# Optimization experiments

Measured on AMD Instinct MI355X. Metric: run time of the kernel, lower is better.

## Reference

```python
import jax, jax.numpy as jnp
import numpy as np

N, F, H, G = 4096, 256, 8, 128  # atoms, filters, heads, groups
D = F // H  # head dim = 32


def setup_inputs() -> dict:
    key = jax.random.key(0)
    ks = jax.random.split(key, 12)
    x = jax.random.normal(ks[0], (N, F), dtype=jnp.float32)
    # sorted group ids in [0, G): block_diag over unique-count blocks == equality mask on sorted ids
    seg = jnp.sort(jax.random.randint(ks[1], (N,), 0, G, dtype=jnp.int32))
    elem_index = jnp.stack([jnp.arange(N, dtype=jnp.int32), seg])  # [2, N]
    s = 1.0 / np.sqrt(F)
    def lin(k):
        kw, kb = jax.random.split(k)
        return (jax.random.normal(kw, (F, F), dtype=jnp.float32) * s,
                jnp.zeros((F,), dtype=jnp.float32))
    Wq, bq = lin(ks[2]); Wk, bk = lin(ks[3]); Wv, bv = lin(ks[4])
    Wo1, bo1 = lin(ks[5]); Wo2, bo2 = lin(ks[6])
    return {"x": x, "elem_index": elem_index,
            "Wq": Wq, "bq": bq, "Wk": Wk, "bk": bk, "Wv": Wv, "bv": bv,
            "Wo1": Wo1, "bo1": bo1, "Wo2": Wo2, "bo2": bo2}


def reference(x, elem_index, Wq, bq, Wk, bk, Wv, bv, Wo1, bo1, Wo2, bo2):
    n = x.shape[0]
    # projections -> [H, N, D]
    q = (x @ Wq.T + bq).reshape(n, H, D).transpose(1, 0, 2)
    k = (x @ Wk.T + bk).reshape(n, H, D).transpose(1, 0, 2)
    v = (x @ Wv.T + bv).reshape(n, H, D).transpose(1, 0, 2)
    attn = jnp.einsum('hnd,hmd->hnm', q, k)          # [H, N, N]
    attn = jax.nn.silu(attn)                          # attn_act = activation() in source
    seg = elem_index[1]
    mask = (seg[:, None] == seg[None, :]).astype(attn.dtype)  # block-diagonal (sorted ids)
    attn = attn * mask
    out = jnp.einsum('hnm,hmd->hnd', attn, v)        # [H, N, D]
    out = out.transpose(1, 0, 2).reshape(n, F)       # [N, F]
    out = out @ Wo1.T + bo1
    out = jax.ops.segment_sum(out, seg, num_segments=G)  # scatter sum by group -> [G, F]
    out = out @ Wo2.T + bo2
    return jax.nn.silu(out)
```

## Files before the change

kernel.cpp:

```cpp
#include <hip/hip_runtime.h>
#include <math.h>

#define NATOMS 4096
#define FDIM   256
#define NHEAD  8
#define DHEAD  32
#define NGRP   128

typedef __bf16 bf16x8 __attribute__((ext_vector_type(8)));
typedef float  floatx4 __attribute__((ext_vector_type(4)));

__device__ __forceinline__ float silu_f(float x) {
    return x / (1.0f + __expf(-x));
}

__device__ __forceinline__ bf16x8 cvt8(const float* __restrict__ p) {
    float4 f0 = *(const float4*)p;
    float4 f1 = *(const float4*)(p + 4);
    bf16x8 r;
    r[0] = (__bf16)f0.x; r[1] = (__bf16)f0.y; r[2] = (__bf16)f0.z; r[3] = (__bf16)f0.w;
    r[4] = (__bf16)f1.x; r[5] = (__bf16)f1.y; r[6] = (__bf16)f1.z; r[7] = (__bf16)f1.w;
    return r;
}

__global__ __launch_bounds__(256) void k1_qkv_a2(
    const float* __restrict__ x, const int* __restrict__ seg,
    const float* __restrict__ Wq, const float* __restrict__ Wk, const float* __restrict__ Wv,
    const float* __restrict__ bq, const float* __restrict__ bk, const float* __restrict__ bv,
    const float* __restrict__ Wo1, const float* __restrict__ bo1,
    const float* __restrict__ Wo2,
    float* __restrict__ qkv, float* __restrict__ A2, float* __restrict__ c1,
    float* __restrict__ cntf, int* __restrict__ off)
{
    __shared__ float As[32][33];
    __shared__ float Bs[32][33];
    __shared__ int   segs[NATOMS];

    const int tid = threadIdx.x;
    const int bid = blockIdx.x;

    if (bid < 512) {
        int lane = tid & 63;
        int ww = tid >> 6;
        int wrow = ww >> 1, wcol = ww & 1;
        int tm = bid & 63;
        int tn = bid >> 6;
        int m_base = tm * 64 + wrow * 32;
        int n_base = tn * 96 + wcol * 48;

        int l15 = lane & 15;
        int quad = lane >> 4;
        int kq = quad * 8;

        floatx4 acc[2][3] = {};

        const float* arow0 = x + (size_t)(m_base + l15) * 256 + kq;
        const float* arow1 = arow0 + 16 * 256;
        const float* brow[3];
        const float* bias[3];
#pragma unroll
        for (int ni = 0; ni < 3; ++ni) {
            int col = n_base + ni * 16 + l15;
            int w = col >> 8, c = col & 255;
            const float* W = (w == 0) ? Wq : (w == 1) ? Wk : Wv;
            brow[ni] = W + (size_t)c * 256 + kq;
            bias[ni] = ((w == 0) ? bq : (w == 1) ? bk : bv) + c;
        }

#pragma unroll
        for (int ks = 0; ks < 8; ++ks) {
            int ko = ks * 32;
            bf16x8 a0 = cvt8(arow0 + ko);
            bf16x8 a1 = cvt8(arow1 + ko);
#pragma unroll
            for (int ni = 0; ni < 3; ++ni) {
                bf16x8 b = cvt8(brow[ni] + ko);
                acc[0][ni] = __builtin_amdgcn_mfma_f32_16x16x32_bf16(a0, b, acc[0][ni], 0, 0, 0);
                acc[1][ni] = __builtin_amdgcn_mfma_f32_16x16x32_bf16(a1, b, acc[1][ni], 0, 0, 0);
            }
        }

#pragma unroll
        for (int mi = 0; mi < 2; ++mi) {
#pragma unroll
            for (int ni = 0; ni < 3; ++ni) {
                int col = n_base + ni * 16 + l15;
                int w = col >> 8, c = col & 255;
                float bb = *bias[ni];
                float* outp = qkv + (size_t)w * ((size_t)NATOMS * FDIM) + c;
#pragma unroll
                for (int r = 0; r < 4; ++r) {
                    int row = m_base + mi * 16 + quad * 4 + r;
                    outp[(size_t)row * FDIM] = acc[mi][ni][r] + bb;
                }
            }
        }
    } else if (bid < 576) {
        int t = bid - 512;
        int i0 = (t >> 3) * 32;
        int j0 = (t & 7) * 32;
        bool do_c1 = (t & 7) == 0;
        int tx = tid & 15;
        int ty = tid >> 4;
        int lm = tid >> 3;
        int lk = (tid & 7) << 2;

        float acc[2][2] = {};
        float c1acc = 0.0f;

        for (int kt = 0; kt < 256; kt += 32) {
            const float4 av = *(const float4*)(Wo2 + (size_t)(i0 + lm) * 256 + kt + lk);
            const float4 bv = *(const float4*)(Wo1 + (size_t)(kt + lm) * 256 + j0 + lk);
            As[lk + 0][lm] = av.x; As[lk + 1][lm] = av.y;
            As[lk + 2][lm] = av.z; As[lk + 3][lm] = av.w;
            Bs[lm][lk + 0] = bv.x; Bs[lm][lk + 1] = bv.y;
            Bs[lm][lk + 2] = bv.z; Bs[lm][lk + 3] = bv.w;
            __syncthreads();

#pragma unroll
            for (int kk = 0; kk < 32; ++kk) {
                float a0 = As[kk][ty * 2], a1 = As[kk][ty * 2 + 1];
                float b0 = Bs[kk][tx * 2], b1 = Bs[kk][tx * 2 + 1];
                acc[0][0] = fmaf(a0, b0, acc[0][0]);
                acc[0][1] = fmaf(a0, b1, acc[0][1]);
                acc[1][0] = fmaf(a1, b0, acc[1][0]);
                acc[1][1] = fmaf(a1, b1, acc[1][1]);
            }
            if (do_c1) {
                float4 bb = *(const float4*)(bo1 + kt + lk);
                c1acc = fmaf(As[lk + 0][lm], bb.x, c1acc);
                c1acc = fmaf(As[lk + 1][lm], bb.y, c1acc);
                c1acc = fmaf(As[lk + 2][lm], bb.z, c1acc);
                c1acc = fmaf(As[lk + 3][lm], bb.w, c1acc);
            }
            __syncthreads();
        }

#pragma unroll
        for (int i = 0; i < 2; ++i)
#pragma unroll
            for (int j = 0; j < 2; ++j)
                A2[(size_t)(i0 + ty * 2 + i) * 256 + j0 + tx * 2 + j] = acc[i][j];

        if (do_c1) {
            c1acc += __shfl_xor(c1acc, 1, 8);
            c1acc += __shfl_xor(c1acc, 2, 8);
            c1acc += __shfl_xor(c1acc, 4, 8);
            if ((tid & 7) == 0) c1[i0 + lm] = c1acc;
        }
    } else {
        for (int i = tid; i < NATOMS; i += 256) segs[i] = seg[i];
        __syncthreads();
        if (tid < NGRP) {
            int g = tid;
            auto lb = [&](int val) {
                int lo = 0, hi = NATOMS;
                while (lo < hi) {
                    int mid = (lo + hi) >> 1;
                    if (segs[mid] < val) lo = mid + 1; else hi = mid;
                }
                return lo;
            };
            int a = lb(g);
            int b = lb(g + 1);
            off[g] = a;
            if (g == NGRP - 1) off[NGRP] = NATOMS;
            cntf[g] = (float)(b - a);
        }
    }
}

__global__ __launch_bounds__(256) void attn_kernel(
    const float* __restrict__ qkv, const int* __restrict__ off,
    float* __restrict__ Ysum)
{
    int g = blockIdx.x, h = blockIdx.y;
    int base = off[g];
    int end  = off[g + 1];
    base = min(max(base, 0), NATOMS);
    end  = min(max(end, base), NATOMS);
    int n = end - base;

    __shared__ float4 qt4[64 * 8];
    __shared__ float4 vt4[32 * 8];
    __shared__ float  wred[8][32];
    __shared__ float  w[32];
    __shared__ float  red[8][32];

    int tid = threadIdx.x;
    int jj = tid & 31;
    int iq = tid >> 5;
    int d = tid & 31;
    int r = tid >> 5;

    const float* q = qkv;
    const float* k = qkv + (size_t)NATOMS * FDIM;
    const float* v = qkv + 2 * (size_t)NATOMS * FDIM;

    const float4* q4 = (const float4*)(q + (size_t)base * FDIM) + h * 8;
    const float4* k4 = (const float4*)(k + (size_t)base * FDIM) + h * 8;
    const float4* v4 = (const float4*)(v + (size_t)base * FDIM) + h * 8;

    float accY = 0.0f;

    for (int j0 = 0; j0 < n; j0 += 32) {
        int jt_n = min(32, n - j0);
        __syncthreads();
        for (int idx = tid; idx < jt_n * 8; idx += 256)
            vt4[idx] = v4[(size_t)(j0 + (idx >> 3)) * 64 + (idx & 7)];

        float4 kr[8];
        {
            int jrow = (jj < jt_n) ? (j0 + jj) : j0;
#pragma unroll
            for (int c = 0; c < 8; ++c) kr[c] = k4[(size_t)jrow * 64 + c];
        }

        float wpart = 0.0f;
        for (int i0 = 0; i0 < n; i0 += 64) {
            int it_n = min(64, n - i0);
            __syncthreads();
            for (int idx = tid; idx < it_n * 8; idx += 256)
                qt4[idx] = q4[(size_t)(i0 + (idx >> 3)) * 64 + (idx & 7)];
            __syncthreads();
            if (jj < jt_n) {
                for (int ii = iq; ii < it_n; ii += 8) {
                    const float4* qr = &qt4[ii * 8];
                    float s = 0.0f;
#pragma unroll
                    for (int c = 0; c < 8; ++c) {
                        float4 a = qr[c];
                        s = fmaf(a.x, kr[c].x, s);
                        s = fmaf(a.y, kr[c].y, s);
                        s = fmaf(a.z, kr[c].z, s);
                        s = fmaf(a.w, kr[c].w, s);
                    }
                    wpart += silu_f(s);
                }
            }
        }
        wred[iq][jj] = wpart;
        __syncthreads();
        if (tid < 32) {
            float s = 0.0f;
#pragma unroll
            for (int rr = 0; rr < 8; ++rr) s += wred[rr][tid];
            w[tid] = s;
        }
        __syncthreads();
        const float* vts = (const float*)vt4;
        for (int j = r; j < jt_n; j += 8)
            accY = fmaf(w[j], vts[j * 32 + d], accY);
    }

    red[r][d] = accY;
    __syncthreads();
    if (r == 0) {
        float s = 0.0f;
#pragma unroll
        for (int rr = 0; rr < 8; ++rr) s += red[rr][d];
        Ysum[(size_t)g * FDIM + h * DHEAD + d] = s;
    }
}

__global__ __launch_bounds__(256) void k3_tail(
    const float* __restrict__ Ysum, const float* __restrict__ A2,
    const float* __restrict__ c1, const float* __restrict__ bo2,
    const float* __restrict__ cntf, float* __restrict__ out)
{
    __shared__ float As[32][17];
    __shared__ float Bs[32][33];

    int tid = threadIdx.x;
    int bm = (blockIdx.x >> 3) * 16;
    int bn = (blockIdx.x & 7) * 32;
    int tx = tid & 15;
    int ty = tid >> 4;

    float acc0 = 0.0f, acc1 = 0.0f;

    for (int kt = 0; kt < 256; kt += 32) {
        if (tid < 128) {
            int row = tid >> 3, kq = (tid & 7) << 2;
            const float4 av = *(const float4*)(Ysum + (size_t)(bm + row) * 256 + kt + kq);
            As[kq + 0][row] = av.x; As[kq + 1][row] = av.y;
            As[kq + 2][row] = av.z; As[kq + 3][row] = av.w;
        }
        {
            int row = tid >> 3, kq = (tid & 7) << 2;
            const float4 bv = *(const float4*)(A2 + (size_t)(bn + row) * 256 + kt + kq);
            Bs[kq + 0][row] = bv.x; Bs[kq + 1][row] = bv.y;
            Bs[kq + 2][row] = bv.z; Bs[kq + 3][row] = bv.w;
        }
        __syncthreads();

#pragma unroll
        for (int kk = 0; kk < 32; ++kk) {
            float a = As[kk][ty];
            acc0 = fmaf(a, Bs[kk][tx * 2], acc0);
            acc1 = fmaf(a, Bs[kk][tx * 2 + 1], acc1);
        }
        __syncthreads();
    }

    int m = bm + ty;
    float cnt = cntf[m];
    int n0 = bn + tx * 2;
    float v0 = silu_f(acc0 + cnt * c1[n0] + bo2[n0]);
    float v1 = silu_f(acc1 + cnt * c1[n0 + 1] + bo2[n0 + 1]);
    out[(size_t)m * 256 + n0] = v0;
    out[(size_t)m * 256 + n0 + 1] = v1;
}

extern "C" void kernel_launch(void* const* d_in, const int* in_sizes, int n_in,
                              void* d_out, int out_size, void* d_ws, size_t ws_size,
                              hipStream_t stream) {
    const float* x    = (const float*)d_in[0];
    const int*   eidx = (const int*)  d_in[1];
    const float* Wq   = (const float*)d_in[2];
    const float* bq   = (const float*)d_in[3];
    const float* Wk   = (const float*)d_in[4];
    const float* bk   = (const float*)d_in[5];
    const float* Wv   = (const float*)d_in[6];
    const float* bv   = (const float*)d_in[7];
    const float* Wo1  = (const float*)d_in[8];
    const float* bo1  = (const float*)d_in[9];
    const float* Wo2  = (const float*)d_in[10];
    const float* bo2  = (const float*)d_in[11];
    float* out = (float*)d_out;

    const int* seg = eidx + NATOMS;

    const size_t NF = (size_t)NATOMS * FDIM;
    const size_t GF = (size_t)NGRP * FDIM;

    float* qkv  = (float*)d_ws;
    float* Ysum = qkv + 3 * NF;
    float* A2   = Ysum + GF;
    float* c1   = A2 + 256 * 256;
    float* cntf = c1 + 256;
    int*   off  = (int*)(cntf + NGRP);

    k1_qkv_a2<<<577, 256, 0, stream>>>(x, seg, Wq, Wk, Wv, bq, bk, bv,
                                       Wo1, bo1, Wo2, qkv, A2, c1, cntf, off);

    dim3 gattn(NGRP, NHEAD);
    attn_kernel<<<gattn, 256, 0, stream>>>(qkv, off, Ysum);

    k3_tail<<<64, 256, 0, stream>>>(Ysum, A2, c1, bo2, cntf, out);
}
```

Before: 131.7 us.

## Fuse QKV, attention and tail kernels into one launch with atomic flags

Merges the three kernel launches into a single kernel. Role is chosen by block index, and stages are ordered with agent-scope atomic counters and spin-waits rather than kernel boundaries. Attention work is packed four group/head jobs per block so all blocks can be co-resident. This removes inter-kernel launch gaps and lets the A2 work overlap the attention stage. The costs are less attention parallelism per block and a risk of deadlock or races: the F_READY flag is never reset between calls, so on repeated launches producer blocks can signal before the counters are cleared.

```diff
diff --git a/kernel.cpp b/kernel.cpp
--- a/kernel.cpp
+++ b/kernel.cpp
@@ -6,6 +6,20 @@
 #define NHEAD  8
 #define DHEAD  32
 #define NGRP   128
+
+#define NB_QKV   512
+#define NB_A2    64
+#define B_OFF    (NB_QKV + NB_A2)
+#define B_ATTN0  (B_OFF + 1)
+#define NB_ATTN  256
+#define B_TAIL0  (B_ATTN0 + NB_ATTN)
+#define NB_TAIL  64
+#define NB_ALL   (B_TAIL0 + NB_TAIL)
+
+#define F_READY  0
+#define F_QKV    16
+#define F_A2     32
+#define F_ATTN   48
 
 typedef __bf16 bf16x8 __attribute__((ext_vector_type(8)));
 typedef float  floatx4 __attribute__((ext_vector_type(4)));
@@ -23,23 +37,46 @@
     return r;
 }
 
-__global__ __launch_bounds__(256) void k1_qkv_a2(
+__device__ __forceinline__ void wait_eq(int* p, int val) {
+    while (__hip_atomic_load(p, __ATOMIC_ACQUIRE, __HIP_MEMORY_SCOPE_AGENT) != val)
+        __builtin_amdgcn_s_sleep(2);
+}
+
+__device__ __forceinline__ void signal_add(int* p) {
+    __hip_atomic_fetch_add(p, 1, __ATOMIC_RELEASE, __HIP_MEMORY_SCOPE_AGENT);
+}
+
+struct SM {
+    union {
+        struct {
+            float4 qt4[64 * 8];
+            float4 vt4[32 * 8];
+            float  wred[8][32];
+            float  w[32];
+            float  red[8][32];
+        } a;
+        int segs[NATOMS];
+        struct { float As[32][33]; float Bs[32][33]; } g;
+        struct { float As[32][17]; float Bs[32][33]; } t;
+    };
+};
+
+__global__ __launch_bounds__(256, 4) void fused_all(
     const float* __restrict__ x, const int* __restrict__ seg,
     const float* __restrict__ Wq, const float* __restrict__ Wk, const float* __restrict__ Wv,
     const float* __restrict__ bq, const float* __restrict__ bk, const float* __restrict__ bv,
     const float* __restrict__ Wo1, const float* __restrict__ bo1,
-    const float* __restrict__ Wo2,
-    float* __restrict__ qkv, float* __restrict__ A2, float* __restrict__ c1,
-    float* __restrict__ cntf, int* __restrict__ off)
+    const float* __restrict__ Wo2, const float* __restrict__ bo2,
+    float* __restrict__ out,
+    float* __restrict__ qkv, float* __restrict__ Ysum,
+    float* __restrict__ A2, float* __restrict__ c1,
+    float* __restrict__ cntf, int* __restrict__ off, int* __restrict__ flags)
 {
-    __shared__ float As[32][33];
-    __shared__ float Bs[32][33];
-    __shared__ int   segs[NATOMS];
-
+    __shared__ SM sm;
     const int tid = threadIdx.x;
     const int bid = blockIdx.x;
 
-    if (bid < 512) {
+    if (bid < NB_QKV) {
         int lane = tid & 63;
         int ww = tid >> 6;
         int wrow = ww >> 1, wcol = ww & 1;
@@ -95,8 +132,12 @@
                 }
             }
         }
-    } else if (bid < 576) {
-        int t = bid - 512;
+        __threadfence();
+        __syncthreads();
+        if (tid == 0) { wait_eq(&flags[F_READY], 1); signal_add(&flags[F_QKV]); }
+
+    } else if (bid < B_OFF) {
+        int t = bid - NB_QKV;
         int i0 = (t >> 3) * 32;
         int j0 = (t & 7) * 32;
         bool do_c1 = (t & 7) == 0;
@@ -111,16 +152,16 @@
         for (int kt = 0; kt < 256; kt += 32) {
             const float4 av = *(const float4*)(Wo2 + (size_t)(i0 + lm) * 256 + kt + lk);
             const float4 bv = *(const float4*)(Wo1 + (size_t)(kt + lm) * 256 + j0 + lk);
-            As[lk + 0][lm] = av.x; As[lk + 1][lm] = av.y;
-            As[lk + 2][lm] = av.z; As[lk + 3][lm] = av.w;
-            Bs[lm][lk + 0] = bv.x; Bs[lm][lk + 1] = bv.y;
-            Bs[lm][lk + 2] = bv.z; Bs[lm][lk + 3] = bv.w;
+            sm.g.As[lk + 0][lm] = av.x; sm.g.As[lk + 1][lm] = av.y;
+            sm.g.As[lk + 2][lm] = av.z; sm.g.As[lk + 3][lm] = av.w;
+            sm.g.Bs[lm][lk + 0] = bv.x; sm.g.Bs[lm][lk + 1] = bv.y;
+            sm.g.Bs[lm][lk + 2] = bv.z; sm.g.Bs[lm][lk + 3] = bv.w;
             __syncthreads();
 
 #pragma unroll
             for (int kk = 0; kk < 32; ++kk) {
-                float a0 = As[kk][ty * 2], a1 = As[kk][ty * 2 + 1];
-                float b0 = Bs[kk][tx * 2], b1 = Bs[kk][tx * 2 + 1];
+                float a0 = sm.g.As[kk][ty * 2], a1 = sm.g.As[kk][ty * 2 + 1];
+                float b0 = sm.g.Bs[kk][tx * 2], b1 = sm.g.Bs[kk][tx * 2 + 1];
                 acc[0][0] = fmaf(a0, b0, acc[0][0]);
                 acc[0][1] = fmaf(a0, b1, acc[0][1]);
                 acc[1][0] = fmaf(a1, b0, acc[1][0]);
@@ -128,10 +169,10 @@
             }
             if (do_c1) {
                 float4 bb = *(const float4*)(bo1 + kt + lk);
-                c1acc = fmaf(As[lk + 0][lm], bb.x, c1acc);
-                c1acc = fmaf(As[lk + 1][lm], bb.y, c1acc);
-                c1acc = fmaf(As[lk + 2][lm], bb.z, c1acc);
-                c1acc = fmaf(As[lk + 3][lm], bb.w, c1acc);
+                c1acc = fmaf(sm.g.As[lk + 0][lm], bb.x, c1acc);
+                c1acc = fmaf(sm.g.As[lk + 1][lm], bb.y, c1acc);
+                c1acc = fmaf(sm.g.As[lk + 2][lm], bb.z, c1acc);
+                c1acc = fmaf(sm.g.As[lk + 3][lm], bb.w, c1acc);
             }
             __syncthreads();
         }
@@ -148,8 +189,15 @@
             c1acc += __shfl_xor(c1acc, 4, 8);
             if ((tid & 7) == 0) c1[i0 + lm] = c1acc;
         }
-    } else {
-        for (int i = tid; i < NATOMS; i += 256) segs[i] = seg[i];
+        __threadfence();
+        __syncthreads();
+        if (tid == 0) { wait_eq(&flags[F_READY], 1); signal_add(&flags[F_A2]); }
+
+    } else if (bid == B_OFF) {
+        if (tid == 1) flags[F_QKV] = 0;
+        if (tid == 2) flags[F_A2] = 0;
+        if (tid == 3) flags[F_ATTN] = 0;
+        for (int i = tid; i < NATOMS; i += 256) sm.segs[i] = seg[i];
         __syncthreads();
         if (tid < NGRP) {
             int g = tid;
@@ -157,7 +205,7 @@
                 int lo = 0, hi = NATOMS;
                 while (lo < hi) {
                     int mid = (lo + hi) >> 1;
-                    if (segs[mid] < val) lo = mid + 1; else hi = mid;
+                    if (sm.segs[mid] < val) lo = mid + 1; else hi = mid;
                 }
                 return lo;
             };
@@ -167,149 +215,149 @@
             if (g == NGRP - 1) off[NGRP] = NATOMS;
             cntf[g] = (float)(b - a);
         }
+        __threadfence();
+        __syncthreads();
+        if (tid == 0)
+            __hip_atomic_store(&flags[F_READY], 1, __ATOMIC_RELEASE, __HIP_MEMORY_SCOPE_AGENT);
+
+    } else if (bid < B_TAIL0) {
+        if (tid == 0) wait_eq(&flags[F_QKV], NB_QKV);
+        __syncthreads();
+
+        const float* q = qkv;
+        const float* k = qkv + (size_t)NATOMS * FDIM;
+        const float* v = qkv + 2 * (size_t)NATOMS * FDIM;
+
+        int jj = tid & 31;
+        int iq = tid >> 5;
+        int d = tid & 31;
+        int r = tid >> 5;
+
+        for (int t = 0; t < 4; ++t) {
+            int job = (bid - B_ATTN0) * 4 + t;
+            int g = job >> 3, h = job & 7;
+
+            int base = off[g];
+            int end  = off[g + 1];
+            base = min(max(base, 0), NATOMS);
+            end  = min(max(end, base), NATOMS);
+            int n = end - base;
+
+            const float4* q4 = (const float4*)(q + (size_t)base * FDIM) + h * 8;
+            const float4* k4 = (const float4*)(k + (size_t)base * FDIM) + h * 8;
+            const float4* v4 = (const float4*)(v + (size_t)base * FDIM) + h * 8;
+
+            float accY = 0.0f;
+
+            for (int j0 = 0; j0 < n; j0 += 32) {
+                int jt_n = min(32, n - j0);
+                __syncthreads();
+                for (int idx = tid; idx < jt_n * 8; idx += 256)
+                    sm.a.vt4[idx] = v4[(size_t)(j0 + (idx >> 3)) * 64 + (idx & 7)];
+
+                float4 kr[8];
+                {
+                    int jrow = (jj < jt_n) ? (j0 + jj) : j0;
+#pragma unroll
+                    for (int c = 0; c < 8; ++c) kr[c] = k4[(size_t)jrow * 64 + c];
+                }
+
+                float wpart = 0.0f;
+                for (int i0 = 0; i0 < n; i0 += 64) {
+                    int it_n = min(64, n - i0);
+                    __syncthreads();
+                    for (int idx = tid; idx < it_n * 8; idx += 256)
+                        sm.a.qt4[idx] = q4[(size_t)(i0 + (idx >> 3)) * 64 + (idx & 7)];
+                    __syncthreads();
+                    if (jj < jt_n) {
+                        for (int ii = iq; ii < it_n; ii += 8) {
+                            const float4* qr = &sm.a.qt4[ii * 8];
+                            float s = 0.0f;
+#pragma unroll
+                            for (int c = 0; c < 8; ++c) {
+                                float4 a = qr[c];
+                                s = fmaf(a.x, kr[c].x, s);
+                                s = fmaf(a.y, kr[c].y, s);
+                                s = fmaf(a.z, kr[c].z, s);
+                                s = fmaf(a.w, kr[c].w, s);
+                            }
+                            wpart += silu_f(s);
+                        }
+                    }
+                }
+                sm.a.wred[iq][jj] = wpart;
+                __syncthreads();
+                if (tid < 32) {
+                    float s = 0.0f;
+#pragma unroll
+                    for (int rr = 0; rr < 8; ++rr) s += sm.a.wred[rr][tid];
+                    sm.a.w[tid] = s;
+                }
+                __syncthreads();
+                const float* vts = (const float*)sm.a.vt4;
+                for (int j = r; j < jt_n; j += 8)
+                    accY = fmaf(sm.a.w[j], vts[j * 32 + d], accY);
+            }
+
+            sm.a.red[r][d] = accY;
+            __syncthreads();
+            if (r == 0) {
+                float s = 0.0f;
+#pragma unroll
+                for (int rr = 0; rr < 8; ++rr) s += sm.a.red[rr][d];
+                Ysum[(size_t)g * FDIM + h * DHEAD + d] = s;
+            }
+            __syncthreads();
+        }
+        __threadfence();
+        __syncthreads();
+        if (tid == 0) signal_add(&flags[F_ATTN]);
+
+    } else {
+        if (tid == 0) {
+            wait_eq(&flags[F_ATTN], NB_ATTN);
+            wait_eq(&flags[F_A2], NB_A2);
+        }
+        __syncthreads();
+
+        int blk = bid - B_TAIL0;
+        int bm = (blk >> 3) * 16;
+        int bn = (blk & 7) * 32;
+        int tx = tid & 15;
+        int ty = tid >> 4;
+
+        float acc0 = 0.0f, acc1 = 0.0f;
+
+        for (int kt = 0; kt < 256; kt += 32) {
+            if (tid < 128) {
+                int row = tid >> 3, kq = (tid & 7) << 2;
+                const float4 av = *(const float4*)(Ysum + (size_t)(bm + row) * 256 + kt + kq);
+                sm.t.As[kq + 0][row] = av.x; sm.t.As[kq + 1][row] = av.y;
+                sm.t.As[kq + 2][row] = av.z; sm.t.As[kq + 3][row] = av.w;
+            }
+            {
+                int row = tid >> 3, kq = (tid & 7) << 2;
+                const float4 bv = *(const float4*)(A2 + (size_t)(bn + row) * 256 + kt + kq);
+                sm.t.Bs[kq + 0][row] = bv.x; sm.t.Bs[kq + 1][row] = bv.y;
+                sm.t.Bs[kq + 2][row] = bv.z; sm.t.Bs[kq + 3][row] = bv.w;
+            }
+            __syncthreads();
+
+#pragma unroll
+            for (int kk = 0; kk < 32; ++kk) {
+                float a = sm.t.As[kk][ty];
+                acc0 = fmaf(a, sm.t.Bs[kk][tx * 2], acc0);
+                acc1 = fmaf(a, sm.t.Bs[kk][tx * 2 + 1], acc1);
+            }
+            __syncthreads();
+        }
+
+        int m = bm + ty;
+        float cnt = cntf[m];
+        int n0 = bn + tx * 2;
+        out[(size_t)m * 256 + n0]     = silu_f(acc0 + cnt * c1[n0] + bo2[n0]);
+        out[(size_t)m * 256 + n0 + 1] = silu_f(acc1 + cnt * c1[n0 + 1] + bo2[n0 + 1]);
     }
-}
-
-__global__ __launch_bounds__(256) void attn_kernel(
-    const float* __restrict__ qkv, const int* __restrict__ off,
-    float* __restrict__ Ysum)
-{
-    int g = blockIdx.x, h = blockIdx.y;
-    int base = off[g];
-    int end  = off[g + 1];
-    base = min(max(base, 0), NATOMS);
-    end  = min(max(end, base), NATOMS);
-    int n = end - base;
-
-    __shared__ float4 qt4[64 * 8];
-    __shared__ float4 vt4[32 * 8];
-    __shared__ float  wred[8][32];
-    __shared__ float  w[32];
-    __shared__ float  red[8][32];
-
-    int tid = threadIdx.x;
-    int jj = tid & 31;
-    int iq = tid >> 5;
-    int d = tid & 31;
-    int r = tid >> 5;
-
-    const float* q = qkv;
-    const float* k = qkv + (size_t)NATOMS * FDIM;
-    const float* v = qkv + 2 * (size_t)NATOMS * FDIM;
-
-    const float4* q4 = (const float4*)(q + (size_t)base * FDIM) + h * 8;
-    const float4* k4 = (const float4*)(k + (size_t)base * FDIM) + h * 8;
-    const float4* v4 = (const float4*)(v + (size_t)base * FDIM) + h * 8;
-
-    float accY = 0.0f;
-
-    for (int j0 = 0; j0 < n; j0 += 32) {
-        int jt_n = min(32, n - j0);
-        __syncthreads();
-        for (int idx = tid; idx < jt_n * 8; idx += 256)
-            vt4[idx] = v4[(size_t)(j0 + (idx >> 3)) * 64 + (idx & 7)];
-
-        float4 kr[8];
-        {
-            int jrow = (jj < jt_n) ? (j0 + jj) : j0;
-#pragma unroll
-            for (int c = 0; c < 8; ++c) kr[c] = k4[(size_t)jrow * 64 + c];
-        }
-
-        float wpart = 0.0f;
-        for (int i0 = 0; i0 < n; i0 += 64) {
-            int it_n = min(64, n - i0);
-            __syncthreads();
-            for (int idx = tid; idx < it_n * 8; idx += 256)
-                qt4[idx] = q4[(size_t)(i0 + (idx >> 3)) * 64 + (idx & 7)];
-            __syncthreads();
-            if (jj < jt_n) {
-                for (int ii = iq; ii < it_n; ii += 8) {
-                    const float4* qr = &qt4[ii * 8];
-                    float s = 0.0f;
-#pragma unroll
-                    for (int c = 0; c < 8; ++c) {
-                        float4 a = qr[c];
-                        s = fmaf(a.x, kr[c].x, s);
-                        s = fmaf(a.y, kr[c].y, s);
-                        s = fmaf(a.z, kr[c].z, s);
-                        s = fmaf(a.w, kr[c].w, s);
-                    }
-                    wpart += silu_f(s);
-                }
-            }
-        }
-        wred[iq][jj] = wpart;
-        __syncthreads();
-        if (tid < 32) {
-            float s = 0.0f;
-#pragma unroll
-            for (int rr = 0; rr < 8; ++rr) s += wred[rr][tid];
-            w[tid] = s;
-        }
-        __syncthreads();
-        const float* vts = (const float*)vt4;
-        for (int j = r; j < jt_n; j += 8)
-            accY = fmaf(w[j], vts[j * 32 + d], accY);
-    }
-
-    red[r][d] = accY;
-    __syncthreads();
-    if (r == 0) {
-        float s = 0.0f;
-#pragma unroll
-        for (int rr = 0; rr < 8; ++rr) s += red[rr][d];
-        Ysum[(size_t)g * FDIM + h * DHEAD + d] = s;
-    }
-}
-
-__global__ __launch_bounds__(256) void k3_tail(
-    const float* __restrict__ Ysum, const float* __restrict__ A2,
-    const float* __restrict__ c1, const float* __restrict__ bo2,
-    const float* __restrict__ cntf, float* __restrict__ out)
-{
-    __shared__ float As[32][17];
-    __shared__ float Bs[32][33];
-
-    int tid = threadIdx.x;
-    int bm = (blockIdx.x >> 3) * 16;
-    int bn = (blockIdx.x & 7) * 32;
-    int tx = tid & 15;
-    int ty = tid >> 4;
-
-    float acc0 = 0.0f, acc1 = 0.0f;
-
-    for (int kt = 0; kt < 256; kt += 32) {
-        if (tid < 128) {
-            int row = tid >> 3, kq = (tid & 7) << 2;
-            const float4 av = *(const float4*)(Ysum + (size_t)(bm + row) * 256 + kt + kq);
-            As[kq + 0][row] = av.x; As[kq + 1][row] = av.y;
-            As[kq + 2][row] = av.z; As[kq + 3][row] = av.w;
-        }
-        {
-            int row = tid >> 3, kq = (tid & 7) << 2;
-            const float4 bv = *(const float4*)(A2 + (size_t)(bn + row) * 256 + kt + kq);
-            Bs[kq + 0][row] = bv.x; Bs[kq + 1][row] = bv.y;
-            Bs[kq + 2][row] = bv.z; Bs[kq + 3][row] = bv.w;
-        }
-        __syncthreads();
-
-#pragma unroll
-        for (int kk = 0; kk < 32; ++kk) {
-            float a = As[kk][ty];
-            acc0 = fmaf(a, Bs[kk][tx * 2], acc0);
-            acc1 = fmaf(a, Bs[kk][tx * 2 + 1], acc1);
-        }
-        __syncthreads();
-    }
-
-    int m = bm + ty;
-    float cnt = cntf[m];
-    int n0 = bn + tx * 2;
-    float v0 = silu_f(acc0 + cnt * c1[n0] + bo2[n0]);
-    float v1 = silu_f(acc1 + cnt * c1[n0 + 1] + bo2[n0 + 1]);
-    out[(size_t)m * 256 + n0] = v0;
-    out[(size_t)m * 256 + n0 + 1] = v1;
 }
 
 extern "C" void kernel_launch(void* const* d_in, const int* in_sizes, int n_in,
@@ -334,18 +382,15 @@
     const size_t NF = (size_t)NATOMS * FDIM;
     const size_t GF = (size_t)NGRP * FDIM;
 
-    float* qkv  = (float*)d_ws;
-    float* Ysum = qkv + 3 * NF;
-    float* A2   = Ysum + GF;
-    float* c1   = A2 + 256 * 256;
-    float* cntf = c1 + 256;
-    int*   off  = (int*)(cntf + NGRP);
-
-    k1_qkv_a2<<<577, 256, 0, stream>>>(x, seg, Wq, Wk, Wv, bq, bk, bv,
-                                       Wo1, bo1, Wo2, qkv, A2, c1, cntf, off);
-
-    dim3 gattn(NGRP, NHEAD);
-    attn_kernel<<<gattn, 256, 0, stream>>>(qkv, off, Ysum);
-
-    k3_tail<<<64, 256, 0, stream>>>(Ysum, A2, c1, bo2, cntf, out);
-}
+    float* qkv   = (float*)d_ws;
+    float* Ysum  = qkv + 3 * NF;
+    float* A2    = Ysum + GF;
+    float* c1    = A2 + 256 * 256;
+    float* cntf  = c1 + 256;
+    int*   off   = (int*)(cntf + NGRP);
+    int*   flags = off + 160;
+
+    fused_all<<<NB_ALL, 256, 0, stream>>>(x, seg, Wq, Wk, Wv, bq, bk, bv,
+                                          Wo1, bo1, Wo2, bo2, out,
+                                          qkv, Ysum, A2, c1, cntf, off, flags);
+}
```

Measured after the change: 325.8 us. 147% more time.

## Fuse tail GEMM into attention kernel via last-block-per-group atomic counter

Applied to the files above, without the earlier changes.

Removes the separate k3_tail launch. Each attention block bumps a per-group atomic counter, and the last of the 8 head blocks for a group computes that group's output row. To give this tail coalesced reads, A2 is now stored transposed, and the counters are zeroed in the first kernel. This saves one kernel launch and its dependency gap, at the cost of a serialized matvec (256x256 reads of A2T) in one block per group, plus fences and atomics.

```diff
diff --git a/kernel.cpp b/kernel.cpp
--- a/kernel.cpp
+++ b/kernel.cpp
@@ -29,8 +29,8 @@
     const float* __restrict__ bq, const float* __restrict__ bk, const float* __restrict__ bv,
     const float* __restrict__ Wo1, const float* __restrict__ bo1,
     const float* __restrict__ Wo2,
-    float* __restrict__ qkv, float* __restrict__ A2, float* __restrict__ c1,
-    float* __restrict__ cntf, int* __restrict__ off)
+    float* __restrict__ qkv, float* __restrict__ A2T, float* __restrict__ c1,
+    float* __restrict__ cntf, int* __restrict__ off, int* __restrict__ gcnt)
 {
     __shared__ float As[32][33];
     __shared__ float Bs[32][33];
@@ -140,7 +140,7 @@
         for (int i = 0; i < 2; ++i)
 #pragma unroll
             for (int j = 0; j < 2; ++j)
-                A2[(size_t)(i0 + ty * 2 + i) * 256 + j0 + tx * 2 + j] = acc[i][j];
+                A2T[(size_t)(j0 + tx * 2 + j) * 256 + (i0 + ty * 2 + i)] = acc[i][j];
 
         if (do_c1) {
             c1acc += __shfl_xor(c1acc, 1, 8);
@@ -150,6 +150,7 @@
         }
     } else {
         for (int i = tid; i < NATOMS; i += 256) segs[i] = seg[i];
+        if (tid < NGRP) gcnt[tid] = 0;
         __syncthreads();
         if (tid < NGRP) {
             int g = tid;
@@ -170,9 +171,12 @@
     }
 }
 
-__global__ __launch_bounds__(256) void attn_kernel(
+__global__ __launch_bounds__(256) void attn_tail(
     const float* __restrict__ qkv, const int* __restrict__ off,
-    float* __restrict__ Ysum)
+    float* __restrict__ Ysum, const float* __restrict__ A2T,
+    const float* __restrict__ c1, const float* __restrict__ bo2,
+    const float* __restrict__ cntf, int* __restrict__ gcnt,
+    float* __restrict__ out)
 {
     int g = blockIdx.x, h = blockIdx.y;
     int base = off[g];
@@ -186,6 +190,7 @@
     __shared__ float  wred[8][32];
     __shared__ float  w[32];
     __shared__ float  red[8][32];
+    __shared__ int    lastf;
 
     int tid = threadIdx.x;
     int jj = tid & 31;
@@ -261,55 +266,29 @@
         for (int rr = 0; rr < 8; ++rr) s += red[rr][d];
         Ysum[(size_t)g * FDIM + h * DHEAD + d] = s;
     }
-}
-
-__global__ __launch_bounds__(256) void k3_tail(
-    const float* __restrict__ Ysum, const float* __restrict__ A2,
-    const float* __restrict__ c1, const float* __restrict__ bo2,
-    const float* __restrict__ cntf, float* __restrict__ out)
-{
-    __shared__ float As[32][17];
-    __shared__ float Bs[32][33];
-
-    int tid = threadIdx.x;
-    int bm = (blockIdx.x >> 3) * 16;
-    int bn = (blockIdx.x & 7) * 32;
-    int tx = tid & 15;
-    int ty = tid >> 4;
-
-    float acc0 = 0.0f, acc1 = 0.0f;
-
-    for (int kt = 0; kt < 256; kt += 32) {
-        if (tid < 128) {
-            int row = tid >> 3, kq = (tid & 7) << 2;
-            const float4 av = *(const float4*)(Ysum + (size_t)(bm + row) * 256 + kt + kq);
-            As[kq + 0][row] = av.x; As[kq + 1][row] = av.y;
-            As[kq + 2][row] = av.z; As[kq + 3][row] = av.w;
-        }
-        {
-            int row = tid >> 3, kq = (tid & 7) << 2;
-            const float4 bv = *(const float4*)(A2 + (size_t)(bn + row) * 256 + kt + kq);
-            Bs[kq + 0][row] = bv.x; Bs[kq + 1][row] = bv.y;
-            Bs[kq + 2][row] = bv.z; Bs[kq + 3][row] = bv.w;
-        }
-        __syncthreads();
-
-#pragma unroll
-        for (int kk = 0; kk < 32; ++kk) {
-            float a = As[kk][ty];
-            acc0 = fmaf(a, Bs[kk][tx * 2], acc0);
-            acc1 = fmaf(a, Bs[kk][tx * 2 + 1], acc1);
-        }
-        __syncthreads();
-    }
-
-    int m = bm + ty;
-    float cnt = cntf[m];
-    int n0 = bn + tx * 2;
-    float v0 = silu_f(acc0 + cnt * c1[n0] + bo2[n0]);
-    float v1 = silu_f(acc1 + cnt * c1[n0 + 1] + bo2[n0 + 1]);
-    out[(size_t)m * 256 + n0] = v0;
-    out[(size_t)m * 256 + n0 + 1] = v1;
+
+    __threadfence();
+    __syncthreads();
+    if (tid == 0) {
+        int prev = __hip_atomic_fetch_add(&gcnt[g], 1, __ATOMIC_ACQ_REL,
+                                          __HIP_MEMORY_SCOPE_AGENT);
+        lastf = (prev == NHEAD - 1) ? 1 : 0;
+    }
+    __syncthreads();
+    if (!lastf) return;
+
+    float* ys = (float*)qt4;
+    ys[tid] = __hip_atomic_load(&Ysum[(size_t)g * FDIM + tid],
+                                __ATOMIC_RELAXED, __HIP_MEMORY_SCOPE_AGENT);
+    __syncthreads();
+
+    float s = 0.0f;
+    for (int k0 = 0; k0 < 256; k0 += 8) {
+#pragma unroll
+        for (int kk = 0; kk < 8; ++kk)
+            s = fmaf(ys[k0 + kk], A2T[(size_t)(k0 + kk) * 256 + tid], s);
+    }
+    out[(size_t)g * FDIM + tid] = silu_f(s + cntf[g] * c1[tid] + bo2[tid]);
 }
 
 extern "C" void kernel_launch(void* const* d_in, const int* in_sizes, int n_in,
@@ -336,16 +315,16 @@
 
     float* qkv  = (float*)d_ws;
     float* Ysum = qkv + 3 * NF;
-    float* A2   = Ysum + GF;
-    float* c1   = A2 + 256 * 256;
+    float* A2T  = Ysum + GF;
+    float* c1   = A2T + 256 * 256;
     float* cntf = c1 + 256;
     int*   off  = (int*)(cntf + NGRP);
+    int*   gcnt = off + 160;
 
     k1_qkv_a2<<<577, 256, 0, stream>>>(x, seg, Wq, Wk, Wv, bq, bk, bv,
-                                       Wo1, bo1, Wo2, qkv, A2, c1, cntf, off);
+                                       Wo1, bo1, Wo2, qkv, A2T, c1, cntf, off, gcnt);
 
     dim3 gattn(NGRP, NHEAD);
-    attn_kernel<<<gattn, 256, 0, stream>>>(qkv, off, Ysum);
-
-    k3_tail<<<64, 256, 0, stream>>>(Ysum, A2, c1, bo2, cntf, out);
-}
+    attn_tail<<<gattn, 256, 0, stream>>>(qkv, off, Ysum, A2T, c1, bo2,
+                                         cntf, gcnt, out);
+}
```

Result: slower. 197.7 us (+50.1%).
